# Kernel tuning notes

Measured on AMD Instinct MI355X. Metric: run time of the kernel, lower is better.

## Reference

```python
import jax, jax.numpy as jnp
import numpy as np

N_ENTITY = 100000
N_RELATION = 64
DIM = 16
N_HOP = 2
N_MEM = 32
N_NODES = 16384


def setup_inputs() -> dict:
    key = jax.random.key(0)
    ks = jax.random.split(key, 7)
    return {
        "nodes": jax.random.randint(ks[0], (N_NODES,), 0, N_ENTITY),
        "memories_h": jax.random.randint(ks[1], (N_HOP, N_NODES, N_MEM), 0, N_ENTITY),
        "memories_r": jax.random.randint(ks[2], (N_HOP, N_NODES, N_MEM), 0, N_RELATION),
        "memories_t": jax.random.randint(ks[3], (N_HOP, N_NODES, N_MEM), 0, N_ENTITY),
        "entity_emb": jax.random.normal(ks[4], (N_ENTITY, DIM), jnp.float32) * 0.1,
        "relation_emb": jax.random.normal(ks[5], (N_RELATION, DIM * DIM), jnp.float32) * 0.1,
        "W": jax.random.normal(ks[6], (DIM, DIM), jnp.float32) * 0.1,
    }


def reference(nodes, memories_h, memories_r, memories_t, entity_emb, relation_emb, W):
    # item embeddings for the query nodes: [N, D]
    item = entity_emb[nodes]
    o_list = []
    for hop in range(N_HOP):  # small fixed hop count (2)
        h = entity_emb[memories_h[hop]]                                  # [N, M, D]
        r = relation_emb[memories_r[hop]].reshape(-1, N_MEM, DIM, DIM)   # [N, M, D, D]
        t = entity_emb[memories_t[hop]]                                  # [N, M, D]
        # Rh = R @ h : [N, M, D]
        Rh = jnp.einsum('nmde,nme->nmd', r, h)
        # attention over the n_memory slots (softmax dim=0 per node in original)
        probs = jax.nn.softmax(jnp.einsum('nmd,nd->nm', Rh, item), axis=1)
        # weighted sum of tails: [N, D]
        o = jnp.einsum('nm,nmd->nd', probs, t)
        # item_update_mode == 'plus_transform': Linear(dim, dim, bias=False)
        item = (item + o) @ W.T
        o_list.append(o)
    # Faithful to the original torch in-place semantics: at hop 0 the line
    # `kg_feature += o_list[0]` doubles o0 in place; the final result for
    # n_hop=2 is therefore o1 + 2*o0.
    return o_list[1] + 2.0 * o_list[0]
```

## Files before the change

### kernel.cpp

```cpp
#include <hip/hip_runtime.h>

#define NE     100000
#define NR     64
#define DIM    16
#define NHOP   2
#define NMEM   32
#define NNODES 16384

#define WPITCH 20
#define ET_BYTES (NE * DIM * 2)
#define NB_ET  ((NE * DIM / 4 + 255) / 256)

typedef __attribute__((ext_vector_type(2))) _Float16 half2_t;

static __device__ __forceinline__ half2_t as_h2(unsigned u) {
    union { unsigned i; half2_t h; } c; c.i = u; return c.h;
}
static __device__ __forceinline__ float qdot2(unsigned u, unsigned ip, float q) {
#if __has_builtin(__builtin_amdgcn_fdot2)
    return __builtin_amdgcn_fdot2(as_h2(u), as_h2(ip), q, false);
#else
    half2_t a = as_h2(u), b = as_h2(ip);
    return q + (float)a.x * (float)b.x + (float)a.y * (float)b.y;
#endif
}
static __device__ __forceinline__ float dpp_sum16(float v) {
    union { int i; float f; } a, b;
    a.f = v;
    b.i = __builtin_amdgcn_update_dpp(0, a.i, 0xB1,  0xf, 0xf, true); a.f += b.f;
    b.i = __builtin_amdgcn_update_dpp(0, a.i, 0x4E,  0xf, 0xf, true); a.f += b.f;
    b.i = __builtin_amdgcn_update_dpp(0, a.i, 0x124, 0xf, 0xf, true); a.f += b.f;
    b.i = __builtin_amdgcn_update_dpp(0, a.i, 0x128, 0xf, 0xf, true); a.f += b.f;
    return a.f;
}
static __device__ __forceinline__ float bcast(float v, int l) {
    return __int_as_float(__builtin_amdgcn_readlane(__float_as_int(v), l));
}
static __device__ __forceinline__ unsigned short f2h(float f) {
    union { _Float16 h; unsigned short s; } c; c.h = (_Float16)f; return c.s;
}
static __device__ __forceinline__ unsigned pack2h(float a, float b) {
    union { _Float16 h[2]; unsigned u; } c;
    c.h[0] = (_Float16)a; c.h[1] = (_Float16)b;
    return c.u;
}

extern "C" __global__ void __launch_bounds__(256)
prep_kernel(const float* __restrict__ ent, const float* __restrict__ rel,
            _Float16* __restrict__ et, unsigned short* __restrict__ rtg, int n4)
{
    const int b = blockIdx.x, tid = threadIdx.x;
    if (b < NB_ET) {
        int i = b * 256 + tid;
        if (i < n4) {
            float4 v = ((const float4*)ent)[i];
            union { _Float16 h[4]; unsigned long long u; } c;
            c.h[0] = (_Float16)v.x; c.h[1] = (_Float16)v.y;
            c.h[2] = (_Float16)v.z; c.h[3] = (_Float16)v.w;
            *(unsigned long long*)(et + 4 * (long long)i) = c.u;
        }
    } else {
        int j = (b - NB_ET) * 256 + tid;
        const float4* rel4 = (const float4*)rel;
        #pragma unroll
        for (int k = 0; k < 4; ++k) {
            int vidx = k * 1024 + j;
            float4 v = rel4[vidx];
            int k0 = vidx * 4;
            int r  = k0 >> 8;
            int kk = k0 & 255;
            int d  = kk >> 4;
            int e0 = kk & 15;
            int phys = ((d >> 2) + (e0 >> 2)) & 3;
            unsigned short* p = &rtg[r * 256 + e0 * 16 + phys * 4 + (d & 3)];
            p[0]  = f2h(v.x);
            p[16] = f2h(v.y);
            p[32] = f2h(v.z);
            p[48] = f2h(v.w);
        }
    }
}

extern "C" __global__ void __launch_bounds__(256, 4)
ripple_kernel(const int* __restrict__ nodes,
              const int* __restrict__ mh,
              const int* __restrict__ mr,
              const int* __restrict__ mt,
              const _Float16* __restrict__ et,
              const unsigned short* __restrict__ rtg,
              const float* __restrict__ W,
              float* __restrict__ out)
{
    __shared__ __align__(16) unsigned short rt[NR * 256];
    __shared__ __align__(16) float ws[DIM * WPITCH];

    const int tid  = threadIdx.x;
    const int lane = tid & 63;
    const int wid  = tid >> 6;
    const int g    = lane >> 4;
    const int e    = lane & 15;
    const int n    = blockIdx.x * 4 + wid;

    const int ib0 = 0 * (NNODES * NMEM) + n * NMEM + g * 8;
    const int ib1 = 1 * (NNODES * NMEM) + n * NMEM + g * 8;
    int hi0[8], ri0[8], ti0[8], hi1[8], ri1[8], ti1[8];
    {
        const int4* p;
        p = (const int4*)(mh + ib0); *(int4*)&hi0[0] = p[0]; *(int4*)&hi0[4] = p[1];
        p = (const int4*)(mr + ib0); *(int4*)&ri0[0] = p[0]; *(int4*)&ri0[4] = p[1];
        p = (const int4*)(mt + ib0); *(int4*)&ti0[0] = p[0]; *(int4*)&ti0[4] = p[1];
        p = (const int4*)(mh + ib1); *(int4*)&hi1[0] = p[0]; *(int4*)&hi1[4] = p[1];
        p = (const int4*)(mr + ib1); *(int4*)&ri1[0] = p[0]; *(int4*)&ri1[4] = p[1];
        p = (const int4*)(mt + ib1); *(int4*)&ti1[0] = p[0]; *(int4*)&ti1[4] = p[1];
    }
    const int nd = nodes[n];

    float4 stg[8];
    {
        const float4* src = (const float4*)rtg;
        #pragma unroll
        for (int i = 0; i < 8; ++i) stg[i] = src[i * 256 + tid];
    }
    const float wv = W[tid];

    float item = (float)et[nd * DIM + e];
    float hv0[8], tv0[8], hv1[8], tv1[8];
    #pragma unroll
    for (int it = 0; it < 8; ++it) {
        hv0[it] = (float)et[hi0[it] * DIM + e];
        tv0[it] = (float)et[ti0[it] * DIM + e];
        hv1[it] = (float)et[hi1[it] * DIM + e];
        tv1[it] = (float)et[ti1[it] * DIM + e];
    }

    {
        float4* dst = (float4*)rt;
        #pragma unroll
        for (int i = 0; i < 8; ++i) dst[i * 256 + tid] = stg[i];
        ws[(tid >> 4) * WPITCH + (tid & 15)] = wv;
    }
    __syncthreads();

    int voff[4];
    {
        const int s = e >> 2;
        #pragma unroll
        for (int j = 0; j < 4; ++j)
            voff[j] = e * 32 + (((j + s) & 3) << 3);
    }

    float out_acc = 0.f;

    #pragma unroll
    for (int hop = 0; hop < NHOP; ++hop) {
        const int*   ri = hop ? ri1 : ri0;
        const float* hv = hop ? hv1 : hv0;
        const float* tv = hop ? tv1 : tv0;

        unsigned ip[8];
        #pragma unroll
        for (int j = 0; j < 8; ++j)
            ip[j] = pack2h(bcast(item, 2 * j), bcast(item, 2 * j + 1));

        float Z = 0.f, o = 0.f;
        #pragma unroll
        for (int it = 0; it < 8; ++it) {
            const char* rbase = (const char*)rt + (ri[it] << 9);
            float q = 0.f;
            #pragma unroll
            for (int j = 0; j < 4; ++j) {
                uint2 u = *(const uint2*)(rbase + voff[j]);
                q = qdot2(u.x, ip[2 * j + 0], q);
                q = qdot2(u.y, ip[2 * j + 1], q);
            }
            float sc = dpp_sum16(q * hv[it]);
            float ex = __expf(sc);
            Z += ex;
            o += ex * tv[it];
        }
        Z += __shfl_xor(Z, 16);
        Z += __shfl_xor(Z, 32);
        o += __shfl_xor(o, 16);
        o += __shfl_xor(o, 32);
        o *= 1.f / Z;

        out_acc += (hop == 0) ? 2.f * o : o;

        const float v = item + o;
        float nit = 0.f;
        const float4* wr = (const float4*)&ws[e * WPITCH];
        #pragma unroll
        for (int j = 0; j < 4; ++j) {
            float4 w = wr[j];
            nit += w.x * bcast(v, 4 * j + 0) + w.y * bcast(v, 4 * j + 1)
                 + w.z * bcast(v, 4 * j + 2) + w.w * bcast(v, 4 * j + 3);
        }
        item = nit;
    }

    if (lane < 16) out[n * DIM + e] = out_acc;
}

extern "C" void kernel_launch(void* const* d_in, const int* in_sizes, int n_in,
                              void* d_out, int out_size, void* d_ws, size_t ws_size,
                              hipStream_t stream) {
    const int*   nodes = (const int*)d_in[0];
    const int*   mh    = (const int*)d_in[1];
    const int*   mr    = (const int*)d_in[2];
    const int*   mt    = (const int*)d_in[3];
    const float* ent   = (const float*)d_in[4];
    const float* rel   = (const float*)d_in[5];
    const float* W     = (const float*)d_in[6];
    float*       out   = (float*)d_out;

    _Float16*       et  = (_Float16*)d_ws;
    unsigned short* rtg = (unsigned short*)((char*)d_ws + ET_BYTES);

    const int n4 = NE * DIM / 4;
    prep_kernel<<<NB_ET + 4, 256, 0, stream>>>(ent, rel, et, rtg, n4);

    dim3 grid(NNODES / 4);
    dim3 block(256);
    ripple_kernel<<<grid, block, 0, stream>>>(nodes, mh, mr, mt, et, rtg, W, out);
}
```

Baseline: 100.0 us.

## Process four nodes per wave with prefetched indices for the next node

Result: slower. 103.1 us (+3.1%).

```diff
diff --git a/kernel.cpp b/kernel.cpp
--- a/kernel.cpp
+++ b/kernel.cpp
@@ -99,45 +99,13 @@
     const int wid  = tid >> 6;
     const int g    = lane >> 4;
     const int e    = lane & 15;
-    const int n    = blockIdx.x * 4 + wid;
-
-    const int ib0 = 0 * (NNODES * NMEM) + n * NMEM + g * 8;
-    const int ib1 = 1 * (NNODES * NMEM) + n * NMEM + g * 8;
-    int hi0[8], ri0[8], ti0[8], hi1[8], ri1[8], ti1[8];
-    {
-        const int4* p;
-        p = (const int4*)(mh + ib0); *(int4*)&hi0[0] = p[0]; *(int4*)&hi0[4] = p[1];
-        p = (const int4*)(mr + ib0); *(int4*)&ri0[0] = p[0]; *(int4*)&ri0[4] = p[1];
-        p = (const int4*)(mt + ib0); *(int4*)&ti0[0] = p[0]; *(int4*)&ti0[4] = p[1];
-        p = (const int4*)(mh + ib1); *(int4*)&hi1[0] = p[0]; *(int4*)&hi1[4] = p[1];
-        p = (const int4*)(mr + ib1); *(int4*)&ri1[0] = p[0]; *(int4*)&ri1[4] = p[1];
-        p = (const int4*)(mt + ib1); *(int4*)&ti1[0] = p[0]; *(int4*)&ti1[4] = p[1];
-    }
-    const int nd = nodes[n];
-
-    float4 stg[8];
+
     {
         const float4* src = (const float4*)rtg;
-        #pragma unroll
-        for (int i = 0; i < 8; ++i) stg[i] = src[i * 256 + tid];
-    }
-    const float wv = W[tid];
-
-    float item = (float)et[nd * DIM + e];
-    float hv0[8], tv0[8], hv1[8], tv1[8];
-    #pragma unroll
-    for (int it = 0; it < 8; ++it) {
-        hv0[it] = (float)et[hi0[it] * DIM + e];
-        tv0[it] = (float)et[ti0[it] * DIM + e];
-        hv1[it] = (float)et[hi1[it] * DIM + e];
-        tv1[it] = (float)et[ti1[it] * DIM + e];
-    }
-
-    {
         float4* dst = (float4*)rt;
         #pragma unroll
-        for (int i = 0; i < 8; ++i) dst[i * 256 + tid] = stg[i];
-        ws[(tid >> 4) * WPITCH + (tid & 15)] = wv;
+        for (int i = 0; i < 8; ++i) dst[i * 256 + tid] = src[i * 256 + tid];
+        ws[(tid >> 4) * WPITCH + (tid & 15)] = W[tid];
     }
     __syncthreads();
 
@@ -149,56 +117,112 @@
             voff[j] = e * 32 + (((j + s) & 3) << 3);
     }
 
-    float out_acc = 0.f;
+    const int nbase = blockIdx.x * 16 + wid * 4;
+
+    int4 idx[2][12];
+    int  nd[2];
+
+    {
+        const int n   = nbase;
+        const int ib0 = n * NMEM + g * 8;
+        const int ib1 = NNODES * NMEM + ib0;
+        const int4* p;
+        p = (const int4*)(mh + ib0); idx[0][0] = p[0]; idx[0][1] = p[1];
+        p = (const int4*)(mr + ib0); idx[0][2] = p[0]; idx[0][3] = p[1];
+        p = (const int4*)(mt + ib0); idx[0][4] = p[0]; idx[0][5] = p[1];
+        p = (const int4*)(mh + ib1); idx[0][6] = p[0]; idx[0][7] = p[1];
+        p = (const int4*)(mr + ib1); idx[0][8] = p[0]; idx[0][9] = p[1];
+        p = (const int4*)(mt + ib1); idx[0][10] = p[0]; idx[0][11] = p[1];
+        nd[0] = nodes[n];
+    }
 
     #pragma unroll
-    for (int hop = 0; hop < NHOP; ++hop) {
-        const int*   ri = hop ? ri1 : ri0;
-        const float* hv = hop ? hv1 : hv0;
-        const float* tv = hop ? tv1 : tv0;
-
-        unsigned ip[8];
-        #pragma unroll
-        for (int j = 0; j < 8; ++j)
-            ip[j] = pack2h(bcast(item, 2 * j), bcast(item, 2 * j + 1));
-
-        float Z = 0.f, o = 0.f;
+    for (int i = 0; i < 4; ++i) {
+        const int  cur = i & 1, nxt = cur ^ 1;
+        const int  n   = nbase + i;
+
+        int hi0[8], ri0[8], ti0[8], hi1[8], ri1[8], ti1[8];
+        *(int4*)&hi0[0] = idx[cur][0];  *(int4*)&hi0[4] = idx[cur][1];
+        *(int4*)&ri0[0] = idx[cur][2];  *(int4*)&ri0[4] = idx[cur][3];
+        *(int4*)&ti0[0] = idx[cur][4];  *(int4*)&ti0[4] = idx[cur][5];
+        *(int4*)&hi1[0] = idx[cur][6];  *(int4*)&hi1[4] = idx[cur][7];
+        *(int4*)&ri1[0] = idx[cur][8];  *(int4*)&ri1[4] = idx[cur][9];
+        *(int4*)&ti1[0] = idx[cur][10]; *(int4*)&ti1[4] = idx[cur][11];
+
+        float item = (float)et[nd[cur] * DIM + e];
+        float hv0[8], tv0[8], hv1[8], tv1[8];
         #pragma unroll
         for (int it = 0; it < 8; ++it) {
-            const char* rbase = (const char*)rt + (ri[it] << 9);
-            float q = 0.f;
+            hv0[it] = (float)et[hi0[it] * DIM + e];
+            tv0[it] = (float)et[ti0[it] * DIM + e];
+            hv1[it] = (float)et[hi1[it] * DIM + e];
+            tv1[it] = (float)et[ti1[it] * DIM + e];
+        }
+
+        if (i < 3) {
+            const int n2  = n + 1;
+            const int jb0 = n2 * NMEM + g * 8;
+            const int jb1 = NNODES * NMEM + jb0;
+            const int4* p;
+            p = (const int4*)(mh + jb0); idx[nxt][0] = p[0]; idx[nxt][1] = p[1];
+            p = (const int4*)(mr + jb0); idx[nxt][2] = p[0]; idx[nxt][3] = p[1];
+            p = (const int4*)(mt + jb0); idx[nxt][4] = p[0]; idx[nxt][5] = p[1];
+            p = (const int4*)(mh + jb1); idx[nxt][6] = p[0]; idx[nxt][7] = p[1];
+            p = (const int4*)(mr + jb1); idx[nxt][8] = p[0]; idx[nxt][9] = p[1];
+            p = (const int4*)(mt + jb1); idx[nxt][10] = p[0]; idx[nxt][11] = p[1];
+            nd[nxt] = nodes[n2];
+        }
+
+        float out_acc = 0.f;
+        #pragma unroll
+        for (int hop = 0; hop < NHOP; ++hop) {
+            const int*   ri = hop ? ri1 : ri0;
+            const float* hv = hop ? hv1 : hv0;
+            const float* tv = hop ? tv1 : tv0;
+
+            unsigned ip[8];
+            #pragma unroll
+            for (int j = 0; j < 8; ++j)
+                ip[j] = pack2h(bcast(item, 2 * j), bcast(item, 2 * j + 1));
+
+            float Z = 0.f, o = 0.f;
+            #pragma unroll
+            for (int it = 0; it < 8; ++it) {
+                const char* rbase = (const char*)rt + (ri[it] << 9);
+                float q = 0.f;
+                #pragma unroll
+                for (int j = 0; j < 4; ++j) {
+                    uint2 u = *(const uint2*)(rbase + voff[j]);
+                    q = qdot2(u.x, ip[2 * j + 0], q);
+                    q = qdot2(u.y, ip[2 * j + 1], q);
+                }
+                float sc = dpp_sum16(q * hv[it]);
+                float ex = __expf(sc);
+                Z += ex;
+                o += ex * tv[it];
+            }
+            Z += __shfl_xor(Z, 16);
+            Z += __shfl_xor(Z, 32);
+            o += __shfl_xor(o, 16);
+            o += __shfl_xor(o, 32);
+            o *= 1.f / Z;
+
+            out_acc += (hop == 0) ? 2.f * o : o;
+
+            const float v = item + o;
+            float nit = 0.f;
+            const float4* wr = (const float4*)&ws[e * WPITCH];
             #pragma unroll
             for (int j = 0; j < 4; ++j) {
-                uint2 u = *(const uint2*)(rbase + voff[j]);
-                q = qdot2(u.x, ip[2 * j + 0], q);
-                q = qdot2(u.y, ip[2 * j + 1], q);
+                float4 w = wr[j];
+                nit += w.x * bcast(v, 4 * j + 0) + w.y * bcast(v, 4 * j + 1)
+                     + w.z * bcast(v, 4 * j + 2) + w.w * bcast(v, 4 * j + 3);
             }
-            float sc = dpp_sum16(q * hv[it]);
-            float ex = __expf(sc);
-            Z += ex;
-            o += ex * tv[it];
-        }
-        Z += __shfl_xor(Z, 16);
-        Z += __shfl_xor(Z, 32);
-        o += __shfl_xor(o, 16);
-        o += __shfl_xor(o, 32);
-        o *= 1.f / Z;
-
-        out_acc += (hop == 0) ? 2.f * o : o;
-
-        const float v = item + o;
-        float nit = 0.f;
-        const float4* wr = (const float4*)&ws[e * WPITCH];
-        #pragma unroll
-        for (int j = 0; j < 4; ++j) {
-            float4 w = wr[j];
-            nit += w.x * bcast(v, 4 * j + 0) + w.y * bcast(v, 4 * j + 1)
-                 + w.z * bcast(v, 4 * j + 2) + w.w * bcast(v, 4 * j + 3);
-        }
-        item = nit;
-    }
-
-    if (lane < 16) out[n * DIM + e] = out_acc;
+            item = nit;
+        }
+
+        if (lane < 16) out[n * DIM + e] = out_acc;
+    }
 }
 
 extern "C" void kernel_launch(void* const* d_in, const int* in_sizes, int n_in,
@@ -219,7 +243,7 @@
     const int n4 = NE * DIM / 4;
     prep_kernel<<<NB_ET + 4, 256, 0, stream>>>(ent, rel, et, rtg, n4);
 
-    dim3 grid(NNODES / 4);
+    dim3 grid(NNODES / 16);
     dim3 block(256);
     ripple_kernel<<<grid, block, 0, stream>>>(nodes, mh, mr, mt, et, rtg, W, out);
 }
```

## Map one node per 16-lane group and process four nodes per wavefront

Applied to the files above, without the earlier changes.

Result: no change. 100.5 us (+0.5%).

```diff
diff --git a/kernel.cpp b/kernel.cpp
--- a/kernel.cpp
+++ b/kernel.cpp
@@ -32,9 +32,6 @@
     b.i = __builtin_amdgcn_update_dpp(0, a.i, 0x124, 0xf, 0xf, true); a.f += b.f;
     b.i = __builtin_amdgcn_update_dpp(0, a.i, 0x128, 0xf, 0xf, true); a.f += b.f;
     return a.f;
-}
-static __device__ __forceinline__ float bcast(float v, int l) {
-    return __int_as_float(__builtin_amdgcn_readlane(__float_as_int(v), l));
 }
 static __device__ __forceinline__ unsigned short f2h(float f) {
     union { _Float16 h; unsigned short s; } c; c.h = (_Float16)f; return c.s;
@@ -93,51 +90,20 @@
 {
     __shared__ __align__(16) unsigned short rt[NR * 256];
     __shared__ __align__(16) float ws[DIM * WPITCH];
+    __shared__ __align__(16) float sc32[4][4][16];
 
     const int tid  = threadIdx.x;
     const int lane = tid & 63;
     const int wid  = tid >> 6;
     const int g    = lane >> 4;
     const int e    = lane & 15;
-    const int n    = blockIdx.x * 4 + wid;
-
-    const int ib0 = 0 * (NNODES * NMEM) + n * NMEM + g * 8;
-    const int ib1 = 1 * (NNODES * NMEM) + n * NMEM + g * 8;
-    int hi0[8], ri0[8], ti0[8], hi1[8], ri1[8], ti1[8];
-    {
-        const int4* p;
-        p = (const int4*)(mh + ib0); *(int4*)&hi0[0] = p[0]; *(int4*)&hi0[4] = p[1];
-        p = (const int4*)(mr + ib0); *(int4*)&ri0[0] = p[0]; *(int4*)&ri0[4] = p[1];
-        p = (const int4*)(mt + ib0); *(int4*)&ti0[0] = p[0]; *(int4*)&ti0[4] = p[1];
-        p = (const int4*)(mh + ib1); *(int4*)&hi1[0] = p[0]; *(int4*)&hi1[4] = p[1];
-        p = (const int4*)(mr + ib1); *(int4*)&ri1[0] = p[0]; *(int4*)&ri1[4] = p[1];
-        p = (const int4*)(mt + ib1); *(int4*)&ti1[0] = p[0]; *(int4*)&ti1[4] = p[1];
-    }
-    const int nd = nodes[n];
-
-    float4 stg[8];
+
     {
         const float4* src = (const float4*)rtg;
-        #pragma unroll
-        for (int i = 0; i < 8; ++i) stg[i] = src[i * 256 + tid];
-    }
-    const float wv = W[tid];
-
-    float item = (float)et[nd * DIM + e];
-    float hv0[8], tv0[8], hv1[8], tv1[8];
-    #pragma unroll
-    for (int it = 0; it < 8; ++it) {
-        hv0[it] = (float)et[hi0[it] * DIM + e];
-        tv0[it] = (float)et[ti0[it] * DIM + e];
-        hv1[it] = (float)et[hi1[it] * DIM + e];
-        tv1[it] = (float)et[ti1[it] * DIM + e];
-    }
-
-    {
         float4* dst = (float4*)rt;
         #pragma unroll
-        for (int i = 0; i < 8; ++i) dst[i * 256 + tid] = stg[i];
-        ws[(tid >> 4) * WPITCH + (tid & 15)] = wv;
+        for (int i = 0; i < 8; ++i) dst[i * 256 + tid] = src[i * 256 + tid];
+        ws[(tid >> 4) * WPITCH + (tid & 15)] = W[tid];
     }
     __syncthreads();
 
@@ -149,56 +115,78 @@
             voff[j] = e * 32 + (((j + s) & 3) << 3);
     }
 
+    const int n  = blockIdx.x * 16 + wid * 4 + g;
+    const int nd = nodes[n];
+    float item    = (float)et[nd * DIM + e];
     float out_acc = 0.f;
+
+    const float4* sp = (const float4*)&sc32[wid][g][0];
 
     #pragma unroll
     for (int hop = 0; hop < NHOP; ++hop) {
-        const int*   ri = hop ? ri1 : ri0;
-        const float* hv = hop ? hv1 : hv0;
-        const float* tv = hop ? tv1 : tv0;
-
+        const int ibase = hop * (NNODES * NMEM) + n * NMEM;
+
+        sc32[wid][g][e] = item;
+        float4 f0 = sp[0], f1 = sp[1], f2 = sp[2], f3 = sp[3];
         unsigned ip[8];
-        #pragma unroll
-        for (int j = 0; j < 8; ++j)
-            ip[j] = pack2h(bcast(item, 2 * j), bcast(item, 2 * j + 1));
+        ip[0] = pack2h(f0.x, f0.y); ip[1] = pack2h(f0.z, f0.w);
+        ip[2] = pack2h(f1.x, f1.y); ip[3] = pack2h(f1.z, f1.w);
+        ip[4] = pack2h(f2.x, f2.y); ip[5] = pack2h(f2.z, f2.w);
+        ip[6] = pack2h(f3.x, f3.y); ip[7] = pack2h(f3.z, f3.w);
 
         float Z = 0.f, o = 0.f;
-        #pragma unroll
-        for (int it = 0; it < 8; ++it) {
-            const char* rbase = (const char*)rt + (ri[it] << 9);
-            float q = 0.f;
+
+        #pragma unroll
+        for (int k = 0; k < 4; ++k) {
+            const int mb = ibase + 8 * k;
+            int hi[8], ri[8], ti[8];
+            {
+                const int4* p;
+                p = (const int4*)(mh + mb); *(int4*)&hi[0] = p[0]; *(int4*)&hi[4] = p[1];
+                p = (const int4*)(mr + mb); *(int4*)&ri[0] = p[0]; *(int4*)&ri[4] = p[1];
+                p = (const int4*)(mt + mb); *(int4*)&ti[0] = p[0]; *(int4*)&ti[4] = p[1];
+            }
+            float hv[8], tv[8];
             #pragma unroll
-            for (int j = 0; j < 4; ++j) {
-                uint2 u = *(const uint2*)(rbase + voff[j]);
-                q = qdot2(u.x, ip[2 * j + 0], q);
-                q = qdot2(u.y, ip[2 * j + 1], q);
+            for (int j = 0; j < 8; ++j) {
+                hv[j] = (float)et[hi[j] * DIM + e];
+                tv[j] = (float)et[ti[j] * DIM + e];
             }
-            float sc = dpp_sum16(q * hv[it]);
-            float ex = __expf(sc);
-            Z += ex;
-            o += ex * tv[it];
-        }
-        Z += __shfl_xor(Z, 16);
-        Z += __shfl_xor(Z, 32);
-        o += __shfl_xor(o, 16);
-        o += __shfl_xor(o, 32);
+            #pragma unroll
+            for (int j = 0; j < 8; ++j) {
+                const char* rbase = (const char*)rt + (ri[j] << 9);
+                float q = 0.f;
+                #pragma unroll
+                for (int c = 0; c < 4; ++c) {
+                    uint2 u = *(const uint2*)(rbase + voff[c]);
+                    q = qdot2(u.x, ip[2 * c + 0], q);
+                    q = qdot2(u.y, ip[2 * c + 1], q);
+                }
+                float sc = dpp_sum16(q * hv[j]);
+                float ex = __expf(sc);
+                Z += ex;
+                o += ex * tv[j];
+            }
+        }
         o *= 1.f / Z;
 
-        out_acc += (hop == 0) ? 2.f * o : o;
-
-        const float v = item + o;
-        float nit = 0.f;
-        const float4* wr = (const float4*)&ws[e * WPITCH];
-        #pragma unroll
-        for (int j = 0; j < 4; ++j) {
-            float4 w = wr[j];
-            nit += w.x * bcast(v, 4 * j + 0) + w.y * bcast(v, 4 * j + 1)
-                 + w.z * bcast(v, 4 * j + 2) + w.w * bcast(v, 4 * j + 3);
-        }
-        item = nit;
-    }
-
-    if (lane < 16) out[n * DIM + e] = out_acc;
+        if (hop == 0) {
+            out_acc = 2.f * o;
+            const float v = item + o;
+            sc32[wid][g][e] = v;
+            float4 v0 = sp[0], v1 = sp[1], v2 = sp[2], v3 = sp[3];
+            const float4* wr = (const float4*)&ws[e * WPITCH];
+            float4 w0 = wr[0], w1 = wr[1], w2 = wr[2], w3 = wr[3];
+            item = w0.x * v0.x + w0.y * v0.y + w0.z * v0.z + w0.w * v0.w
+                 + w1.x * v1.x + w1.y * v1.y + w1.z * v1.z + w1.w * v1.w
+                 + w2.x * v2.x + w2.y * v2.y + w2.z * v2.z + w2.w * v2.w
+                 + w3.x * v3.x + w3.y * v3.y + w3.z * v3.z + w3.w * v3.w;
+        } else {
+            out_acc += o;
+        }
+    }
+
+    out[n * DIM + e] = out_acc;
 }
 
 extern "C" void kernel_launch(void* const* d_in, const int* in_sizes, int n_in,
@@ -219,7 +207,7 @@
     const int n4 = NE * DIM / 4;
     prep_kernel<<<NB_ET + 4, 256, 0, stream>>>(ent, rel, et, rtg, n4);
 
-    dim3 grid(NNODES / 4);
+    dim3 grid(NNODES / 16);
     dim3 block(256);
     ripple_kernel<<<grid, block, 0, stream>>>(nodes, mh, mr, mt, et, rtg, W, out);
 }
```
